# Kernel tuning notes

Measured on AMD Instinct MI355X. Metric: run time of the kernel, lower is better.

Reference implementation:

```python
import jax, jax.numpy as jnp
from jax import lax
import numpy as np

FACTOR = 2
KERNEL = 3  # conv kernel size (odd)
DN = ('NCDHW', 'OIDHW', 'NCDHW')


def _setup_fir_kernel():
    # resample_kernel = (1,3,3,1); separable outer product, normalized, * factor**3 gain
    k1 = jnp.asarray([1.0, 3.0, 3.0, 1.0], dtype=jnp.float32)
    k = jnp.einsum('i,j,k->ijk', k1, k1, k1)
    k = k / jnp.sum(k)
    return k * (FACTOR ** 3)  # [4,4,4]


def _upfirdn3d_1x1(x, k, pad0, pad1):
    # upfirdn3d with up=down=1: pad then depthwise-correlate with flipped FIR kernel
    # (torch code runs F.conv3d with torch.flip(kernel)).
    n, c = x.shape[0], x.shape[1]
    xp = jnp.pad(x, ((0, 0), (0, 0), (pad0, pad1), (pad0, pad1), (pad0, pad1)))
    kf = jnp.flip(k).astype(x.dtype)  # flip all 3 spatial axes
    w = jnp.broadcast_to(kf[None, None], (c, 1) + k.shape)  # depthwise [C,1,4,4,4]
    return lax.conv_general_dilated(xp, w, (1, 1, 1), 'VALID',
                                    dimension_numbers=DN,
                                    feature_group_count=c)


def _upsample_conv_3d(x, weight):
    # Equivalent of upsample_conv_3d(x, w, k=(1,3,3,1), factor=2):
    # torch flips the weight and feeds conv_transpose3d(stride=2); the flip and
    # the implicit transpose-flip cancel, so it equals an lhs-dilated correlation
    # with the ORIGINAL weight, padded by (k-1) on each side (output_padding=0).
    k = _setup_fir_kernel()
    p = k.shape[0] - FACTOR - (KERNEL - 1)  # = 0
    pad_lo, pad_hi = (p + 1) // 2 + FACTOR - 1, p // 2 + 1  # = (1, 1)
    y = lax.conv_general_dilated(
        x, weight.astype(x.dtype), (1, 1, 1),
        padding=[(KERNEL - 1, KERNEL - 1)] * 3,
        lhs_dilation=(FACTOR, FACTOR, FACTOR),
        dimension_numbers=DN)  # [N, outC, 33, 33, 33]
    return _upfirdn3d_1x1(y, k, pad_lo, pad_hi)  # [N, outC, 32, 32, 32]


def setup_inputs() -> dict:
    key = jax.random.key(0)
    k1, k2, k3 = jax.random.split(key, 3)
    x = jax.random.normal(k1, (8, 256, 16, 16, 16), dtype=jnp.float32)
    weight = jax.random.normal(k2, (128, 256, 3, 3, 3), dtype=jnp.float32) * 0.05
    bias = jax.random.normal(k3, (128,), dtype=jnp.float32) * 0.05
    return {"x": x, "weight": weight, "bias": bias}


def reference(x, weight, bias):
    y = _upsample_conv_3d(x, weight)
    return y + bias.reshape(1, -1, 1, 1, 1)
```

## Files before the change

### kernel.cpp

```cpp
#include <hip/hip_runtime.h>
#include <string.h>

typedef __attribute__((ext_vector_type(4))) float f32x4;
typedef __attribute__((ext_vector_type(8))) _Float16 f16x8;
typedef unsigned short u16;
typedef unsigned int   u32;

#define NBATCH 8
#define ICN 256
#define OCN 128
#define VOLP 36432
#define WRE 884736
#define XTE 8388608
#define ZBF 4096
#define S1POOL 33792

__host__ __device__ constexpr int cls_yoff2(int c){
  return (c==0)?0:(c==1)?5168:(c==2)?9792:(c==3)?14416:
         (c==4)?18768:(c==5)?23632:(c==6)?27984:32336;
}
__host__ __device__ constexpr int cls_nxyp(int c){
  return ((c&3)==0)?304:((c&3)==3)?256:272;
}

__device__ __forceinline__ u16 f2h(float v){
  _Float16 h = (_Float16)v;
  u16 u; memcpy(&u, &h, 2);
  return u;
}
__device__ __forceinline__ float h2f(u16 u){
  _Float16 h; memcpy(&h, &u, 2);
  return (float)h;
}

#define GLOAD16(gp, lp)                                                        \
  __builtin_amdgcn_global_load_lds(                                            \
      (const __attribute__((address_space(1))) void*)(gp),                     \
      (__attribute__((address_space(3))) void*)(lp), 16, 0, 0)

__global__ __launch_bounds__(256) void prep_w(const float* __restrict__ w,
                                              u16* __restrict__ wh,
                                              float* __restrict__ zb){
  if (blockIdx.x < 16) zb[blockIdx.x*256 + threadIdx.x] = 0.f;
  int idx = blockIdx.x*256 + threadIdx.x;
  int e = idx&7, ln=(idx>>3)&63, og=(idx>>9)&7, icc=(idx>>12)&7, tt=idx>>15;
  int oc = og*16 + (ln&15);
  int ic = icc*32 + ((ln>>4)&3)*8 + e;
  const int toffs[8] = {0,8,12,16,18,22,24,26};
  const int tcnt[8]  = {8,4,4,2,4,2,2,1};
  int c=0, t=0;
  #pragma unroll
  for (int cc=0; cc<8; ++cc)
    if (tt>=toffs[cc] && tt<toffs[cc]+tcnt[cc]){ c=cc; t=tt-toffs[cc]; }
  int ez=c>>2, ey=(c>>1)&1, ex=c&1;
  int ty=2-ey, tx=2-ex;
  int ax=t%tx, ay=(t/tx)%ty, az=t/(tx*ty);
  int qz = ez?1:(az?2:0), qy = ey?1:(ay?2:0), qx = ex?1:(ax?2:0);
  wh[idx] = f2h(w[((size_t)oc*ICN + ic)*27 + (qz*3+qy)*3+qx]);
}

__global__ __launch_bounds__(256) void prep_x(const float* __restrict__ x,
                                              u16* __restrict__ xh){
  u32 o = blockIdx.x*256 + threadIdx.x;
  int il = o & 31, p = (o>>5)&4095, icc = (o>>17)&7, n = o>>20;
  xh[o] = f2h(x[(size_t)(n*256 + icc*32 + il)*4096 + p]);
}

#define S1_ISSUE(BUFBYTE, ICCV, AZV)                                           \
  {                                                                            \
    _Pragma("unroll")                                                          \
    for (int j_=0; j_<3; ++j_){                                                \
      const int r_ = j_*64 + ln;                                               \
      if (r_ < 170){                                                           \
        const int s_ = wv*170 + r_;                                            \
        const int icg_ = s_&3, pos_ = s_>>2;                                   \
        const int xi_ = pos_%17, yi_ = pos_/17;                                \
        const int zc_ = EZ ? mz : (mz-1+(AZV));                                \
        const int yc_ = my0 + yi_ + (EY-1);                                    \
        const int xc_ = xi_ + (EX-1);                                          \
        const bool inb_ = (u32)zc_<16u && (u32)yc_<16u && (u32)xc_<16u;        \
        const size_t g_ = nbase + (size_t)(ICCV)*131072                        \
                        + (size_t)((zc_*256+yc_*16+xc_)*32 + icg_*8);          \
        const u16* gh_ = inb_ ? (xh+g_) : zb16;                                \
        char* lh_ = pool + (BUFBYTE) + s_*16;                                  \
        GLOAD16(gh_, lh_);                                                     \
      }                                                                        \
    }                                                                          \
  }

template<int EZ,int EY,int EX>
__device__ __forceinline__ void s1body(char* pool,
                                       const u16* __restrict__ xh,
                                       const u16* __restrict__ wh,
                                       const u16* __restrict__ zb16,
                                       u16* __restrict__ yd, int n0, int mt, int mz, int nl, int tid)
{
  constexpr int TZ=2-EZ, TY=2-EY, TX=2-EX;
  constexpr int DX=17-EX;
  constexpr int DY=17-EY;
  constexpr int NXY=DY*DX;
  constexpr int CLS = EZ*4+EY*2+EX;
  constexpr int YOFF = cls_yoff2(CLS);
  constexpr int NXYP = cls_nxyp(CLS);
  constexpr int W27 = (CLS==0)?0:(CLS==1)?8:(CLS==2)?12:(CLS==3)?16:
                      (CLS==4)?18:(CLS==5)?22:(CLS==6)?24:26;
  constexpr int NST = TZ*8;
  u16* AsU = (u16*)pool;

  const int wv=tid>>6, ln=tid&63;
  const int mhalf = wv&1, ochalf = wv>>1;
  const int my0=(mt*128)/DX;

  int posA[4];
  #pragma unroll
  for (int fi=0; fi<4; ++fi){
    int m = mt*128 + mhalf*64 + fi*16 + (ln&15);
    if (m > NXY-1) m = NXY-1;
    int my=m/DX, mx=m-my*DX;
    posA[fi] = ((my-my0)*17 + mx)*32 + (ln>>4)*8;
  }

  f32x4 acc[4][4];
  #pragma unroll
  for (int i=0;i<4;++i)
    #pragma unroll
    for (int j=0;j<4;++j) acc[i][j]=(f32x4){0.f,0.f,0.f,0.f};

  const size_t nbase = (size_t)(n0+nl)*(ICN*4096);

  S1_ISSUE(0, 0, 0);

  int st = 0;
  #pragma unroll 1
  for (int icc=0; icc<8; ++icc){
    #pragma unroll
    for (int az=0; az<TZ; ++az){
      const int cur = st & 1;
      const bool have_next = (st+1) < NST;
      if (have_next){
        const int nicc = (az+1<TZ)?icc:(icc+1);
        const int naz  = (az+1<TZ)?(az+1):0;
        S1_ISSUE((cur^1)*10880, nicc, naz);
        asm volatile("s_waitcnt vmcnt(3)" ::: "memory");
      } else {
        asm volatile("s_waitcnt vmcnt(0)" ::: "memory");
      }
      asm volatile("s_barrier" ::: "memory");
      const int curo = cur*5440;

      #pragma unroll
      for (int ay=0; ay<TY; ++ay)
      #pragma unroll
      for (int ax=0; ax<TX; ++ax){
        const int t = (az*TY+ay)*TX+ax;
        const int toff = (ay*17+ax)*32;
        f16x8 ah[4];
        #pragma unroll
        for (int fi=0; fi<4; ++fi)
          ah[fi] = *(const f16x8*)&AsU[curo + posA[fi]+toff];
        const u16* bp = wh + (size_t)(((W27+t)*8+icc)*8)*512 + (ochalf*4)*512 + ln*8;
        f16x8 bh[4];
        #pragma unroll
        for (int og=0; og<4; ++og) bh[og] = *(const f16x8*)(bp + og*512);
        #pragma unroll
        for (int fi=0; fi<4; ++fi)
          #pragma unroll
          for (int og=0; og<4; ++og)
            acc[fi][og] = __builtin_amdgcn_mfma_f32_16x16x32_f16(ah[fi], bh[og], acc[fi][og],0,0,0);
      }
      asm volatile("s_barrier" ::: "memory");
      ++st;
    }
  }

  float* tr = (float*)pool + wv*(64*33);
  #pragma unroll
  for (int pass=0; pass<2; ++pass){
    #pragma unroll
    for (int fi=0; fi<2; ++fi)
      #pragma unroll
      for (int og=0; og<4; ++og)
        #pragma unroll
        for (int j=0; j<4; ++j)
          tr[(og*16+(ln&15))*33 + fi*16 + (ln>>4)*4 + j] = acc[pass*2+fi][og][j];
    int m = mt*128 + mhalf*64 + pass*32 + (ln&31);
    bool valid = m < NXY;
    size_t lbase = (size_t)YOFF + (size_t)mz*NXYP + (valid ? m : 0);
    #pragma unroll 4
    for (int i=0; i<32; ++i){
      int r = 2*i + (ln>>5);
      u16 v = f2h(tr[r*33 + (ln&31)]);
      int oc = ochalf*64 + r;
      if (valid)
        __builtin_nontemporal_store(v, yd + (size_t)(nl*128 + oc)*VOLP + lbase);
    }
  }
}

__global__ __launch_bounds__(256,3) void stage1f(const u16* __restrict__ xh,
                                                 const u16* __restrict__ wh,
                                                 const u16* __restrict__ zb16,
                                                 u16* __restrict__ yd, int n0){
  __shared__ __align__(16) char pool[S1POOL];
  int bid = blockIdx.x, nl, tid = threadIdx.x;
  if (gridDim.z == 1){ nl = bid & 7; bid >>= 3; }
  else               { nl = blockIdx.z; }
  int mz, sub;
  if (bid < 352){ mz = bid/22; sub = bid - mz*22; }
  else          { mz = 16;     sub = bid - 352;   }
  if      (sub <  3) s1body<0,0,0>(pool,xh,wh,zb16,yd,n0,sub   ,mz,nl,tid);
  else if (sub <  6) s1body<0,0,1>(pool,xh,wh,zb16,yd,n0,sub- 3,mz,nl,tid);
  else if (sub <  9) s1body<0,1,0>(pool,xh,wh,zb16,yd,n0,sub- 6,mz,nl,tid);
  else if (sub < 11) s1body<0,1,1>(pool,xh,wh,zb16,yd,n0,sub- 9,mz,nl,tid);
  else if (sub < 14) s1body<1,0,0>(pool,xh,wh,zb16,yd,n0,sub-11,mz,nl,tid);
  else if (sub < 17) s1body<1,0,1>(pool,xh,wh,zb16,yd,n0,sub-14,mz,nl,tid);
  else if (sub < 20) s1body<1,1,0>(pool,xh,wh,zb16,yd,n0,sub-17,mz,nl,tid);
  else               s1body<1,1,1>(pool,xh,wh,zb16,yd,n0,sub-20,mz,nl,tid);
}

__global__ __launch_bounds__(256) void stage2d(const u16* __restrict__ yd, const float* __restrict__ bias,
                                               float* __restrict__ out, int n0){
  __shared__ float raw[33][36];
  __shared__ float fx[35][36];
  const int tid=threadIdx.x;
  const int zg=blockIdx.x, oc=blockIdx.y, nl=blockIdx.z;
  const u16* yb = yd + (size_t)(nl*128+oc)*VOLP;
  const float b = bias[oc];
  float* ob = out + (size_t)((n0+nl)*128+oc)*32768;
  for (int t2=tid; t2<1188; t2+=256) raw[t2/36][t2%36] = 0.f;
  for (int t2=tid; t2<1260; t2+=256) fx[t2/36][t2%36] = 0.f;
  __syncthreads();
  float a0[2][2]={{0,0},{0,0}}, a1[2][2]={{0,0},{0,0}}, a2[2][2]={{0,0},{0,0}};

  #pragma unroll 1
  for (int s=0; s<11; ++s){
    int uz = zg*8 - 1 + s;
    if ((u32)uz < 33u){
      const int cz = uz & 1, zi2 = uz >> 1;
      #pragma unroll 1
      for (int ch=tid; ch<273; ch+=256){
        #define GATH(CY,CX,CHL)                                                     \
        {                                                                           \
          constexpr int DXc = 17-(CX);                                              \
          constexpr int NXYc = (17-(CY))*DXc;                                       \
          constexpr int O0 = cls_yoff2((CY)*2+(CX));                                \
          constexpr int O1 = cls_yoff2(4+(CY)*2+(CX));                              \
          constexpr int PS = cls_nxyp((CY)*2+(CX));                                 \
          const int s2 = 4*(CHL);                                                   \
          const int r0 = s2/DXc;                                                    \
          const int c0 = s2 - r0*DXc;                                               \
          const u16* sp = yb + (cz?O1:O0) + zi2*PS + s2;                            \
          ushort4 v = *(const ushort4*)sp;                                          \
          u16 ve[4] = {v.x, v.y, v.z, v.w};                                         \
          _Pragma("unroll")                                                         \
          for (int e=0; e<4; ++e){                                                  \
            int c = c0+e, rr = r0;                                                  \
            if (c >= DXc){ c -= DXc; rr += 1; }                                     \
            if (s2+e < NXYc) raw[2*rr+(CY)][2*c+(CX)+1] = h2f(ve[e]);               \
          }                                                                         \
        }
        if      (ch <  73) GATH(0,0,ch)
        else if (ch < 141) GATH(0,1,ch-73)
        else if (ch < 209) GATH(1,0,ch-141)
        else               GATH(1,1,ch-209)
        #undef GATH
      }
    } else {
      for (int t2=tid; t2<1188; t2+=256) raw[t2/36][t2%36] = 0.f;
    }
    __syncthreads();
    #pragma unroll 1
    for (int t2=tid; t2<528; t2+=256){
      int uy = t2>>4, j = t2&15;
      float2 A = *(const float2*)&raw[uy][2*j];
      float2 B = *(const float2*)&raw[uy][2*j+2];
      float  Cv = raw[uy][2*j+4];
      float f0 = 0.25f*A.x + 0.75f*A.y + 0.75f*B.x + 0.25f*B.y;
      float f1 = 0.25f*A.y + 0.75f*B.x + 0.75f*B.y + 0.25f*Cv;
      *(float2*)&fx[uy+1][2*j] = make_float2(f0, f1);
    }
    __syncthreads();
    #pragma unroll
    for (int ss=0; ss<2; ++ss){
      int t2 = tid + ss*256;
      int i = t2>>5, ox = t2&31;
      float f0 = fx[2*i  ][ox];
      float f1 = fx[2*i+1][ox];
      float f2 = fx[2*i+2][ox];
      float f3 = fx[2*i+3][ox];
      float f4 = fx[2*i+4][ox];
      float fv0 = 0.25f*f0 + 0.75f*f1 + 0.75f*f2 + 0.25f*f3;
      float fv1 = 0.25f*f1 + 0.75f*f2 + 0.75f*f3 + 0.25f*f4;
      if (s >= 3){
        int oz = zg*8 + s - 3;
        __builtin_nontemporal_store(a0[ss][0] + 0.25f*fv0 + b, ob + (size_t)oz*1024 + (2*i  )*32 + ox);
        __builtin_nontemporal_store(a0[ss][1] + 0.25f*fv1 + b, ob + (size_t)oz*1024 + (2*i+1)*32 + ox);
      }
      a0[ss][0] = a1[ss][0] + 0.75f*fv0;  a1[ss][0] = a2[ss][0] + 0.75f*fv0;  a2[ss][0] = 0.25f*fv0;
      a0[ss][1] = a1[ss][1] + 0.75f*fv1;  a1[ss][1] = a2[ss][1] + 0.75f*fv1;  a2[ss][1] = 0.25f*fv1;
    }
    __syncthreads();
  }
}

extern "C" void kernel_launch(void* const* d_in, const int* in_sizes, int n_in,
                              void* d_out, int out_size, void* d_ws, size_t ws_size,
                              hipStream_t stream) {
  const float* x    = (const float*)d_in[0];
  const float* w    = (const float*)d_in[1];
  const float* bias = (const float*)d_in[2];
  float* out = (float*)d_out;

  float* zb = (float*)d_ws;
  u16* wh = (u16*)(zb + ZBF);
  u16* xh = wh + WRE;
  u16* yd = xh + XTE;
  size_t base = (size_t)ZBF*4 + (size_t)(WRE + XTE)*2;

  int nChunk = 1;
  if      (ws_size >= base + (size_t)8*128*VOLP*2) nChunk=8;
  else if (ws_size >= base + (size_t)4*128*VOLP*2) nChunk=4;
  else if (ws_size >= base + (size_t)2*128*VOLP*2) nChunk=2;

  prep_w<<<dim3(WRE/256), 256, 0, stream>>>(w, wh, zb);
  prep_x<<<dim3(XTE/256), 256, 0, stream>>>(x, xh);

  const u16* zb16 = (const u16*)zb;
  if (nChunk == 8){
    stage1f<<<dim3(2904,1,1),256,0,stream>>>(xh,wh,zb16,yd,0);
    stage2d<<<dim3(4,128,8),256,0,stream>>>(yd,bias,out,0);
  } else {
    for (int n0=0; n0<NBATCH; n0+=nChunk){
      stage1f<<<dim3(363,1,nChunk),256,0,stream>>>(xh,wh,zb16,yd,n0);
      stage2d<<<dim3(4,128,nChunk),256,0,stream>>>(yd,bias,out,n0);
    }
  }
}
```

Before: 201.2 us.

## Stage two input-channel chunks per pipeline step and tile prep_x transpose through LDS

The stage-1 loop now loads two 32-channel chunks per double-buffered stage, which halves the number of barrier-separated pipeline steps and doubles the LDS pool. MFMA sections are wrapped in s_setprio to favour compute waves. prep_x is rewritten to transpose through a shared tile so global reads are coalesced and writes are vectorised. The larger LDS footprint may lower occupancy.

```diff
diff --git a/kernel.cpp b/kernel.cpp
--- a/kernel.cpp
+++ b/kernel.cpp
@@ -13,7 +13,7 @@
 #define WRE 884736
 #define XTE 8388608
 #define ZBF 4096
-#define S1POOL 33792
+#define S1POOL 43520
 
 __host__ __device__ constexpr int cls_yoff2(int c){
   return (c==0)?0:(c==1)?5168:(c==2)?9792:(c==3)?14416:
@@ -61,25 +61,46 @@
 
 __global__ __launch_bounds__(256) void prep_x(const float* __restrict__ x,
                                               u16* __restrict__ xh){
-  u32 o = blockIdx.x*256 + threadIdx.x;
-  int il = o & 31, p = (o>>5)&4095, icc = (o>>17)&7, n = o>>20;
-  xh[o] = f2h(x[(size_t)(n*256 + icc*32 + il)*4096 + p]);
-}
-
-#define S1_ISSUE(BUFBYTE, ICCV, AZV)                                           \
+  __shared__ u16 tile[256*33];
+  const int tid = threadIdx.x;
+  const int b = blockIdx.x;
+  const int n = b >> 7, icc = (b >> 4) & 7, pc = b & 15;
+  const float* xb = x + ((size_t)(n*256 + icc*32))*4096 + pc*256;
+  #pragma unroll 4
+  for (int r = 0; r < 32; ++r)
+    tile[tid*33 + r] = f2h(xb[(size_t)r*4096 + tid]);
+  __syncthreads();
+  u16* ob = xh + ((size_t)(n*8 + icc))*131072 + pc*8192;
+  #pragma unroll
+  for (int j = 0; j < 4; ++j){
+    int c = j*256 + tid;
+    int p = c >> 2, il8 = (c & 3)*8;
+    ushort4 lo, hi;
+    lo.x = tile[p*33+il8+0]; lo.y = tile[p*33+il8+1];
+    lo.z = tile[p*33+il8+2]; lo.w = tile[p*33+il8+3];
+    hi.x = tile[p*33+il8+4]; hi.y = tile[p*33+il8+5];
+    hi.z = tile[p*33+il8+6]; hi.w = tile[p*33+il8+7];
+    *(ushort4*)&ob[c*8]     = lo;
+    *(ushort4*)&ob[c*8 + 4] = hi;
+  }
+}
+
+#define S1_ISSUE(BUFBYTE, ICC0, AZV)                                           \
   {                                                                            \
+    const int iccs_ = wv >> 1;                                                 \
     _Pragma("unroll")                                                          \
-    for (int j_=0; j_<3; ++j_){                                                \
+    for (int j_=0; j_<6; ++j_){                                                \
       const int r_ = j_*64 + ln;                                               \
-      if (r_ < 170){                                                           \
-        const int s_ = wv*170 + r_;                                            \
-        const int icg_ = s_&3, pos_ = s_>>2;                                   \
+      if (r_ < 340){                                                           \
+        const int s_ = wv*340 + r_;                                            \
+        const int in_ = s_ - iccs_*680;                                        \
+        const int icg_ = in_&3, pos_ = in_>>2;                                 \
         const int xi_ = pos_%17, yi_ = pos_/17;                                \
         const int zc_ = EZ ? mz : (mz-1+(AZV));                                \
         const int yc_ = my0 + yi_ + (EY-1);                                    \
         const int xc_ = xi_ + (EX-1);                                          \
         const bool inb_ = (u32)zc_<16u && (u32)yc_<16u && (u32)xc_<16u;        \
-        const size_t g_ = nbase + (size_t)(ICCV)*131072                        \
+        const size_t g_ = nbase + (size_t)((ICC0)+iccs_)*131072                \
                         + (size_t)((zc_*256+yc_*16+xc_)*32 + icg_*8);          \
         const u16* gh_ = inb_ ? (xh+g_) : zb16;                                \
         char* lh_ = pool + (BUFBYTE) + s_*16;                                  \
@@ -104,7 +125,7 @@
   constexpr int NXYP = cls_nxyp(CLS);
   constexpr int W27 = (CLS==0)?0:(CLS==1)?8:(CLS==2)?12:(CLS==3)?16:
                       (CLS==4)?18:(CLS==5)?22:(CLS==6)?24:26;
-  constexpr int NST = TZ*8;
+  constexpr int NST = TZ*4;
   u16* AsU = (u16*)pool;
 
   const int wv=tid>>6, ln=tid&63;
@@ -132,42 +153,48 @@
 
   int st = 0;
   #pragma unroll 1
-  for (int icc=0; icc<8; ++icc){
+  for (int ip=0; ip<4; ++ip){
     #pragma unroll
     for (int az=0; az<TZ; ++az){
       const int cur = st & 1;
       const bool have_next = (st+1) < NST;
       if (have_next){
-        const int nicc = (az+1<TZ)?icc:(icc+1);
-        const int naz  = (az+1<TZ)?(az+1):0;
-        S1_ISSUE((cur^1)*10880, nicc, naz);
-        asm volatile("s_waitcnt vmcnt(3)" ::: "memory");
+        const int nip = (az+1<TZ)?ip:(ip+1);
+        const int naz = (az+1<TZ)?(az+1):0;
+        S1_ISSUE((cur^1)*21760, nip*2, naz);
+        asm volatile("s_waitcnt vmcnt(6)" ::: "memory");
       } else {
         asm volatile("s_waitcnt vmcnt(0)" ::: "memory");
       }
       asm volatile("s_barrier" ::: "memory");
-      const int curo = cur*5440;
-
+      const int curo = cur*10880;
+
+      __builtin_amdgcn_s_setprio(1);
       #pragma unroll
-      for (int ay=0; ay<TY; ++ay)
-      #pragma unroll
-      for (int ax=0; ax<TX; ++ax){
-        const int t = (az*TY+ay)*TX+ax;
-        const int toff = (ay*17+ax)*32;
-        f16x8 ah[4];
+      for (int k=0; k<2; ++k){
+        const int icc = ip*2 + k;
         #pragma unroll
-        for (int fi=0; fi<4; ++fi)
-          ah[fi] = *(const f16x8*)&AsU[curo + posA[fi]+toff];
-        const u16* bp = wh + (size_t)(((W27+t)*8+icc)*8)*512 + (ochalf*4)*512 + ln*8;
-        f16x8 bh[4];
+        for (int ay=0; ay<TY; ++ay)
         #pragma unroll
-        for (int og=0; og<4; ++og) bh[og] = *(const f16x8*)(bp + og*512);
-        #pragma unroll
-        for (int fi=0; fi<4; ++fi)
+        for (int ax=0; ax<TX; ++ax){
+          const int t = (az*TY+ay)*TX+ax;
+          const int toff = (ay*17+ax)*32;
+          f16x8 ah[4];
           #pragma unroll
-          for (int og=0; og<4; ++og)
-            acc[fi][og] = __builtin_amdgcn_mfma_f32_16x16x32_f16(ah[fi], bh[og], acc[fi][og],0,0,0);
+          for (int fi=0; fi<4; ++fi)
+            ah[fi] = *(const f16x8*)&AsU[curo + k*5440 + posA[fi]+toff];
+          const u16* bp = wh + (size_t)(((W27+t)*8+icc)*8)*512 + (ochalf*4)*512 + ln*8;
+          f16x8 bh[4];
+          #pragma unroll
+          for (int og=0; og<4; ++og) bh[og] = *(const f16x8*)(bp + og*512);
+          #pragma unroll
+          for (int fi=0; fi<4; ++fi)
+            #pragma unroll
+            for (int og=0; og<4; ++og)
+              acc[fi][og] = __builtin_amdgcn_mfma_f32_16x16x32_f16(ah[fi], bh[og], acc[fi][og],0,0,0);
+        }
       }
+      __builtin_amdgcn_s_setprio(0);
       asm volatile("s_barrier" ::: "memory");
       ++st;
     }
@@ -323,7 +350,7 @@
   else if (ws_size >= base + (size_t)2*128*VOLP*2) nChunk=2;
 
   prep_w<<<dim3(WRE/256), 256, 0, stream>>>(w, wh, zb);
-  prep_x<<<dim3(XTE/256), 256, 0, stream>>>(x, xh);
+  prep_x<<<dim3(1024), 256, 0, stream>>>(x, xh);
 
   const u16* zb16 = (const u16*)zb;
   if (nChunk == 8){
```

Measured after the change: 188.9 us. -6.1%, faster.

## Merge prep kernels with LDS-transposed x conversion and halve stage1 epilogue LDS

Applied to the files above, without the earlier changes.

Replaces the separate prep_w and prep_x launches with one prep_all kernel. Its x path stages a 32-channel by 256-position tile in LDS so that global reads and vectorized fp16 writes are both coalesced, instead of scattered strided reads. The stage1 epilogue now transposes accumulators in two halves of 32 output channels, which lets the shared pool shrink from 33792 to 21760 bytes and may allow more resident blocks per CU. The cost is an extra pass and barrier-free reuse of the smaller transpose buffer in the epilogue.

```diff
diff --git a/kernel.cpp b/kernel.cpp
--- a/kernel.cpp
+++ b/kernel.cpp
@@ -13,7 +13,7 @@
 #define WRE 884736
 #define XTE 8388608
 #define ZBF 4096
-#define S1POOL 33792
+#define S1POOL 21760
 
 __host__ __device__ constexpr int cls_yoff2(int c){
   return (c==0)?0:(c==1)?5168:(c==2)?9792:(c==3)?14416:
@@ -38,32 +38,53 @@
       (const __attribute__((address_space(1))) void*)(gp),                     \
       (__attribute__((address_space(3))) void*)(lp), 16, 0, 0)
 
-__global__ __launch_bounds__(256) void prep_w(const float* __restrict__ w,
-                                              u16* __restrict__ wh,
-                                              float* __restrict__ zb){
-  if (blockIdx.x < 16) zb[blockIdx.x*256 + threadIdx.x] = 0.f;
-  int idx = blockIdx.x*256 + threadIdx.x;
-  int e = idx&7, ln=(idx>>3)&63, og=(idx>>9)&7, icc=(idx>>12)&7, tt=idx>>15;
-  int oc = og*16 + (ln&15);
-  int ic = icc*32 + ((ln>>4)&3)*8 + e;
-  const int toffs[8] = {0,8,12,16,18,22,24,26};
-  const int tcnt[8]  = {8,4,4,2,4,2,2,1};
-  int c=0, t=0;
-  #pragma unroll
-  for (int cc=0; cc<8; ++cc)
-    if (tt>=toffs[cc] && tt<toffs[cc]+tcnt[cc]){ c=cc; t=tt-toffs[cc]; }
-  int ez=c>>2, ey=(c>>1)&1, ex=c&1;
-  int ty=2-ey, tx=2-ex;
-  int ax=t%tx, ay=(t/tx)%ty, az=t/(tx*ty);
-  int qz = ez?1:(az?2:0), qy = ey?1:(ay?2:0), qx = ex?1:(ax?2:0);
-  wh[idx] = f2h(w[((size_t)oc*ICN + ic)*27 + (qz*3+qy)*3+qx]);
-}
-
-__global__ __launch_bounds__(256) void prep_x(const float* __restrict__ x,
-                                              u16* __restrict__ xh){
-  u32 o = blockIdx.x*256 + threadIdx.x;
-  int il = o & 31, p = (o>>5)&4095, icc = (o>>17)&7, n = o>>20;
-  xh[o] = f2h(x[(size_t)(n*256 + icc*32 + il)*4096 + p]);
+__global__ __launch_bounds__(256) void prep_all(const float* __restrict__ x,
+                                                const float* __restrict__ w,
+                                                u16* __restrict__ xh,
+                                                u16* __restrict__ wh,
+                                                float* __restrict__ zb){
+  __shared__ u16 tile[256*33];
+  const int tid = threadIdx.x;
+  const int b = blockIdx.x;
+  if (b < 1024){
+    const int n = b >> 7, icc = (b >> 4) & 7, pc = b & 15;
+    const float* xb = x + ((size_t)(n*256 + icc*32))*4096 + pc*256;
+    #pragma unroll 4
+    for (int r = 0; r < 32; ++r)
+      tile[tid*33 + r] = f2h(xb[(size_t)r*4096 + tid]);
+    __syncthreads();
+    u16* ob = xh + ((size_t)(n*8 + icc))*131072 + pc*8192;
+    #pragma unroll
+    for (int j = 0; j < 4; ++j){
+      int c = j*256 + tid;
+      int p = c >> 2, il8 = (c & 3)*8;
+      ushort4 lo, hi;
+      lo.x = tile[p*33+il8+0]; lo.y = tile[p*33+il8+1];
+      lo.z = tile[p*33+il8+2]; lo.w = tile[p*33+il8+3];
+      hi.x = tile[p*33+il8+4]; hi.y = tile[p*33+il8+5];
+      hi.z = tile[p*33+il8+6]; hi.w = tile[p*33+il8+7];
+      *(ushort4*)&ob[c*8]     = lo;
+      *(ushort4*)&ob[c*8 + 4] = hi;
+    }
+  } else {
+    const int bb = b - 1024;
+    if (bb < 16) zb[bb*256 + tid] = 0.f;
+    int idx = bb*256 + tid;
+    int e = idx&7, ln=(idx>>3)&63, og=(idx>>9)&7, icc=(idx>>12)&7, tt=idx>>15;
+    int oc = og*16 + (ln&15);
+    int ic = icc*32 + ((ln>>4)&3)*8 + e;
+    const int toffs[8] = {0,8,12,16,18,22,24,26};
+    const int tcnt[8]  = {8,4,4,2,4,2,2,1};
+    int c=0, t=0;
+    #pragma unroll
+    for (int cc=0; cc<8; ++cc)
+      if (tt>=toffs[cc] && tt<toffs[cc]+tcnt[cc]){ c=cc; t=tt-toffs[cc]; }
+    int ez=c>>2, ey=(c>>1)&1, ex=c&1;
+    int ty=2-ey, tx=2-ex;
+    int ax=t%tx, ay=(t/tx)%ty, az=t/(tx*ty);
+    int qz = ez?1:(az?2:0), qy = ey?1:(ay?2:0), qx = ex?1:(ax?2:0);
+    wh[idx] = f2h(w[((size_t)oc*ICN + ic)*27 + (qz*3+qy)*3+qx]);
+  }
 }
 
 #define S1_ISSUE(BUFBYTE, ICCV, AZV)                                           \
@@ -173,26 +194,31 @@
     }
   }
 
-  float* tr = (float*)pool + wv*(64*33);
+  float* tr = (float*)pool + wv*(32*33);
   #pragma unroll
-  for (int pass=0; pass<2; ++pass){
-    #pragma unroll
-    for (int fi=0; fi<2; ++fi)
+  for (int h=0; h<2; ++h){
+    #pragma unroll
+    for (int pass=0; pass<2; ++pass){
       #pragma unroll
-      for (int og=0; og<4; ++og)
+      for (int fi=0; fi<2; ++fi)
         #pragma unroll
-        for (int j=0; j<4; ++j)
-          tr[(og*16+(ln&15))*33 + fi*16 + (ln>>4)*4 + j] = acc[pass*2+fi][og][j];
-    int m = mt*128 + mhalf*64 + pass*32 + (ln&31);
-    bool valid = m < NXY;
-    size_t lbase = (size_t)YOFF + (size_t)mz*NXYP + (valid ? m : 0);
-    #pragma unroll 4
-    for (int i=0; i<32; ++i){
-      int r = 2*i + (ln>>5);
-      u16 v = f2h(tr[r*33 + (ln&31)]);
-      int oc = ochalf*64 + r;
-      if (valid)
-        __builtin_nontemporal_store(v, yd + (size_t)(nl*128 + oc)*VOLP + lbase);
+        for (int og2=0; og2<2; ++og2){
+          const int og = h*2 + og2;
+          #pragma unroll
+          for (int j=0; j<4; ++j)
+            tr[(og2*16+(ln&15))*33 + fi*16 + (ln>>4)*4 + j] = acc[pass*2+fi][og][j];
+        }
+      int m = mt*128 + mhalf*64 + pass*32 + (ln&31);
+      bool valid = m < NXY;
+      size_t lbase = (size_t)YOFF + (size_t)mz*NXYP + (valid ? m : 0);
+      #pragma unroll 4
+      for (int i=0; i<16; ++i){
+        int r = 2*i + (ln>>5);
+        u16 v = f2h(tr[r*33 + (ln&31)]);
+        int oc = ochalf*64 + h*32 + r;
+        if (valid)
+          __builtin_nontemporal_store(v, yd + (size_t)(nl*128 + oc)*VOLP + lbase);
+      }
     }
   }
 }
@@ -322,8 +348,7 @@
   else if (ws_size >= base + (size_t)4*128*VOLP*2) nChunk=4;
   else if (ws_size >= base + (size_t)2*128*VOLP*2) nChunk=2;
 
-  prep_w<<<dim3(WRE/256), 256, 0, stream>>>(w, wh, zb);
-  prep_x<<<dim3(XTE/256), 256, 0, stream>>>(x, xh);
+  prep_all<<<dim3(4480), 256, 0, stream>>>(x, w, xh, wh, zb);
 
   const u16* zb16 = (const u16*)zb;
   if (nChunk == 8){
```

After: 188.1 us. 1.07x faster.
